# Optimization experiments

Measured on AMD Instinct MI355X. Metric: run time of the kernel, lower is better.

Reference implementation:

```python
import jax, jax.numpy as jnp
import numpy as np

B, S, C, H = 2, 2048, 2048, 16
Dh = C // H
ROPE_THETA = 10000.0


def _rope(t):
    # t: [B, S, H, Dh]; rotate-half RoPE over head_dim
    half = Dh // 2
    inv_freq = 1.0 / (ROPE_THETA ** (jnp.arange(0, half, dtype=jnp.float32) / half))
    ang = jnp.arange(S, dtype=jnp.float32)[:, None] * inv_freq[None, :]  # [S, half]
    cos = jnp.cos(ang)[None, :, None, :]  # [1,S,1,half]
    sin = jnp.sin(ang)[None, :, None, :]
    t1, t2 = t[..., :half], t[..., half:]
    return jnp.concatenate([t1 * cos - t2 * sin, t2 * cos + t1 * sin], axis=-1)


def setup_inputs() -> dict:
    key = jax.random.key(0)
    k1, k2, k3 = jax.random.split(key, 3)
    x = jax.random.normal(k1, (B, S, C), dtype=jnp.float32)
    Wqkv = jax.random.normal(k2, (C, 3 * C), dtype=jnp.float32) * (C ** -0.5)
    Wproj = jax.random.normal(k3, (C, C), dtype=jnp.float32) * (C ** -0.5)
    return {"x": x, "Wqkv": Wqkv, "Wproj": Wproj}


def reference(x, Wqkv, Wproj):
    batch, seq, hidden = x.shape
    qkv = x @ Wqkv  # [B,S,3C]
    # NOTE: torch code chunks as k, q, v (k first)
    k, q, v = jnp.split(qkv, 3, axis=-1)
    k = k.reshape(batch, seq, H, Dh)
    q = q.reshape(batch, seq, H, Dh)
    v = v.reshape(batch, seq, H, Dh)
    k = _rope(k)
    q = _rope(q)
    scale = Dh ** -0.5
    scores = jnp.einsum('bqhd,bkhd->bhqk', q, k) * scale  # [B,H,S,S]
    causal = jnp.tril(jnp.ones((seq, seq), dtype=bool))
    scores = jnp.where(causal[None, None], scores, jnp.finfo(scores.dtype).min)
    attn = jax.nn.softmax(scores, axis=-1)
    out = jnp.einsum('bhqk,bkhd->bqhd', attn, v).reshape(batch, seq, hidden)
    return out @ Wproj
```

## Files before the change

### kernel.cpp

```cpp
#include <hip/hip_runtime.h>
#include <hip/hip_bf16.h>

#define B_   2
#define S_   2048
#define C_   2048
#define H_   16
#define DH   128
#define C3   (3 * C_)

typedef __attribute__((ext_vector_type(8))) short short8;
typedef __attribute__((ext_vector_type(4))) float floatx4;

__device__ __forceinline__ void gload16(const void* g, void* l) {
  __builtin_amdgcn_global_load_lds(
      (const __attribute__((address_space(1))) unsigned int*)g,
      (__attribute__((address_space(3))) unsigned int*)l, 16, 0, 0);
}

__device__ __forceinline__ unsigned pk_bf16(float a, float b) {
  union { __hip_bfloat16 h; unsigned short u; } ua, ub;
  ua.h = __float2bfloat16(a); ub.h = __float2bfloat16(b);
  return (unsigned)ua.u | ((unsigned)ub.u << 16);
}

__global__ __launch_bounds__(256) void cast_bf16_kernel(
    const float* __restrict__ in, __hip_bfloat16* __restrict__ out, int n4) {
  int i = blockIdx.x * blockDim.x + threadIdx.x;
  if (i >= n4) return;
  float4 v = ((const float4*)in)[i];
  union { __hip_bfloat16 b[4]; uint2 u; } t;
  t.b[0] = __float2bfloat16(v.x);
  t.b[1] = __float2bfloat16(v.y);
  t.b[2] = __float2bfloat16(v.z);
  t.b[3] = __float2bfloat16(v.w);
  ((uint2*)out)[i] = t.u;
}

__global__ __launch_bounds__(256) void transpose_cast_kernel(
    const float* __restrict__ in, __hip_bfloat16* __restrict__ out, int R, int Cc) {
  __shared__ float tile[32][33];
  int c0 = blockIdx.x * 32, r0 = blockIdx.y * 32;
  int tx = threadIdx.x & 31, ty = threadIdx.x >> 5;
#pragma unroll
  for (int k = 0; k < 4; ++k)
    tile[ty + 8 * k][tx] = in[(size_t)(r0 + ty + 8 * k) * Cc + c0 + tx];
  __syncthreads();
#pragma unroll
  for (int k = 0; k < 4; ++k)
    out[(size_t)(c0 + ty + 8 * k) * R + r0 + tx] = __float2bfloat16(tile[tx][ty + 8 * k]);
}


#define S_VMCNT6 do { asm volatile("s_waitcnt vmcnt(6)" ::: "memory"); \
                      __builtin_amdgcn_sched_barrier(0); } while (0)
#define S_LGKM0  do { asm volatile("s_waitcnt lgkmcnt(0)" ::: "memory"); \
                      __builtin_amdgcn_sched_barrier(0); } while (0)
#define S_BAR    do { __builtin_amdgcn_s_barrier(); \
                      __builtin_amdgcn_sched_barrier(0); } while (0)

template <int NCOLS, bool OUT_F32>
__global__ __launch_bounds__(512, 2) void gemm_dp_kernel(
    const __hip_bfloat16* __restrict__ A, const __hip_bfloat16* __restrict__ Bt,
    void* __restrict__ Cp) {
  const int K = 2048, NT = 32;
  __shared__ __hip_bfloat16 lds[3 * 24576];
  const int tid = threadIdx.x;
  const int lane = tid & 63, wv = tid >> 6;
  const int wm = wv >> 1, wn = wv & 1;
  const int lr = lane & 15, lq = lane >> 4;
  const int m0 = blockIdx.y * 256, n0 = blockIdx.x * 128;
  const int sw0 = (lq ^ (lr & 7)) << 3;
  const int sw1 = sw0 ^ 32;

  auto stageA = [&](int bw, int p, int kk) {
    int idx = p * 512 + tid;
    int row = idx >> 3;
    int lc = (idx & 7) ^ (row & 7);
    gload16(A + (size_t)(m0 + row) * K + kk + lc * 8,
            (char*)lds + (size_t)bw * 49152 + (size_t)(p * 512 + wv * 64) * 16);
  };
  auto stageB = [&](int bw, int p, int kk) {
    int idx = p * 512 + tid;
    int row = idx >> 3;
    int lc = (idx & 7) ^ (row & 7);
    gload16(Bt + (size_t)(n0 + row) * K + kk + lc * 8,
            (char*)lds + (size_t)bw * 49152 + 32768 + (size_t)(p * 512 + wv * 64) * 16);
  };

#pragma unroll
  for (int p = 0; p < 4; ++p) stageA(0, p, 0);
#pragma unroll
  for (int p = 0; p < 2; ++p) stageB(0, p, 0);
#pragma unroll
  for (int p = 0; p < 4; ++p) stageA(1, p, 64);
#pragma unroll
  for (int p = 0; p < 2; ++p) stageB(1, p, 64);

  floatx4 acc[4][4] = {};
  int br = 0, bw = 2;

#pragma unroll 1
  for (int t = 0; t < NT; ++t) {
    const int kk2 = (t + 2 < NT) ? (t + 2) * 64 : 0;

    S_VMCNT6;
    S_BAR;

    const __hip_bfloat16* Ab = lds + br * 24576 + (wm * 64 + lr) * 64;
    const __hip_bfloat16* Bb = lds + br * 24576 + 16384 + (wn * 64 + lr) * 64;

    short8 af0[4], bf0[4];
#pragma unroll
    for (int i = 0; i < 4; ++i) af0[i] = *(const short8*)(Ab + i * 1024 + sw0);
#pragma unroll
    for (int j = 0; j < 4; ++j) bf0[j] = *(const short8*)(Bb + j * 1024 + sw0);
    stageA(bw, 0, kk2); stageA(bw, 1, kk2); stageB(bw, 0, kk2);
    S_LGKM0;
    __builtin_amdgcn_s_setprio(1);
#pragma unroll
    for (int i = 0; i < 4; ++i)
#pragma unroll
      for (int j = 0; j < 4; ++j)
        acc[i][j] = __builtin_amdgcn_mfma_f32_16x16x32_bf16(af0[i], bf0[j], acc[i][j], 0, 0, 0);
    __builtin_amdgcn_s_setprio(0);

    short8 af1[4], bf1[4];
#pragma unroll
    for (int i = 0; i < 4; ++i) af1[i] = *(const short8*)(Ab + i * 1024 + sw1);
#pragma unroll
    for (int j = 0; j < 4; ++j) bf1[j] = *(const short8*)(Bb + j * 1024 + sw1);
    stageA(bw, 2, kk2); stageA(bw, 3, kk2); stageB(bw, 1, kk2);
    S_LGKM0;
    __builtin_amdgcn_s_setprio(1);
#pragma unroll
    for (int i = 0; i < 4; ++i)
#pragma unroll
      for (int j = 0; j < 4; ++j)
        acc[i][j] = __builtin_amdgcn_mfma_f32_16x16x32_bf16(af1[i], bf1[j], acc[i][j], 0, 0, 0);
    __builtin_amdgcn_s_setprio(0);

    br = (br == 2) ? 0 : br + 1;
    bw = (bw == 2) ? 0 : bw + 1;
  }

  asm volatile("s_waitcnt vmcnt(0)" ::: "memory");
  __builtin_amdgcn_sched_barrier(0);

#pragma unroll
  for (int i = 0; i < 4; ++i)
#pragma unroll
    for (int j = 0; j < 4; ++j)
#pragma unroll
      for (int r = 0; r < 4; ++r) {
        int row = m0 + wm * 64 + i * 16 + lq * 4 + r;
        int col = n0 + wn * 64 + j * 16 + lr;
        if (OUT_F32)
          ((float*)Cp)[(size_t)row * NCOLS + col] = acc[i][j][r];
        else
          ((__hip_bfloat16*)Cp)[(size_t)row * NCOLS + col] = __float2bfloat16(acc[i][j][r]);
      }
}

__global__ __launch_bounds__(256) void rope_kernel(__hip_bfloat16* __restrict__ qkv) {
  int i = blockIdx.x * blockDim.x + threadIdx.x;
  int d = i & 63;
  int h = (i >> 6) & 15;
  int row = i >> 10;
  int s = row & (S_ - 1);
  float invf = exp2f((float)d * (-13.287712379549449f / 64.0f));
  float ang = (float)s * invf;
  float sn, c;
  __sincosf(ang, &sn, &c);
  size_t base = (size_t)row * C3 + h * DH + d;
  float k1 = __bfloat162float(qkv[base]);
  float k2 = __bfloat162float(qkv[base + 64]);
  qkv[base]      = __float2bfloat16(k1 * c - k2 * sn);
  qkv[base + 64] = __float2bfloat16(k2 * c + k1 * sn);
  const float scale = 0.08838834764831845f * 1.4426950408889634f;
  float q1 = __bfloat162float(qkv[base + C_]);
  float q2 = __bfloat162float(qkv[base + C_ + 64]);
  qkv[base + C_]      = __float2bfloat16((q1 * c - q2 * sn) * scale);
  qkv[base + C_ + 64] = __float2bfloat16((q2 * c + q1 * sn) * scale);
}

__global__ __launch_bounds__(256) void vtrans_kernel(
    const __hip_bfloat16* __restrict__ qkv, __hip_bfloat16* __restrict__ vt) {
  __shared__ short T[64 * 144];
  const int tid = threadIdx.x;
  const int t = blockIdx.x, bh = blockIdx.y;
  const int b = bh >> 4, h = bh & 15;
  const size_t brow = (size_t)b * S_;
#pragma unroll
  for (int p = 0; p < 4; ++p) {
    int idx = p * 256 + tid;
    int row = idx >> 4, c8 = idx & 15;
    *(short8*)(T + row * 144 + c8 * 8) =
        *(const short8*)(qkv + (brow + t * 64 + row) * C3 + 2 * C_ + h * DH + c8 * 8);
  }
  __syncthreads();
#pragma unroll
  for (int p = 0; p < 4; ++p) {
    int L = p * 256 + tid;
    int d = L & 127, cs = L >> 7;
    short8 v;
#pragma unroll
    for (int j = 0; j < 8; ++j) v[j] = T[(cs * 8 + j) * 144 + d];
    *(short8*)(vt + ((size_t)bh * 32 + t) * 8192 + (size_t)L * 8) = v;
  }
}

__global__ __launch_bounds__(256, 2) void attn_kernel(
    const __hip_bfloat16* __restrict__ qkv,
    const __hip_bfloat16* __restrict__ vt_tiles,
    __hip_bfloat16* __restrict__ outp) {
  __shared__ __hip_bfloat16 Ks[64 * 128];
  __shared__ __hip_bfloat16 Vt[64 * 128];
  __shared__ __hip_bfloat16 Ps[4 * 32 * 72];

  const int tid = threadIdx.x, lane = tid & 63, wv = tid >> 6;
  const int lr = lane & 15, lq = lane >> 4;
  const int qt = gridDim.x - 1 - blockIdx.x;
  const int bh = blockIdx.y;
  const int b = bh >> 4, h = bh & 15;
  const int q0 = qt * 128;
  const int q0w = q0 + wv * 32;
  const size_t brow = (size_t)b * S_;

  short8 qf[2][4];
#pragma unroll
  for (int rt = 0; rt < 2; ++rt)
#pragma unroll
    for (int ks = 0; ks < 4; ++ks)
      qf[rt][ks] = *(const short8*)(qkv + (brow + q0w + rt * 16 + lr) * C3 + C_ + h * DH + ks * 32 + lq * 8);

  floatx4 of[2][8] = {};
  float l_run[2] = {0.0f, 0.0f};

  const int wrow_last = q0w + 31;
  const int nkt = 2 * qt + 2;
  for (int kt = 0; kt < nkt; ++kt) {
    const int kb = kt * 64;
#pragma unroll
    for (int p = 0; p < 4; ++p) {
      int L = p * 256 + wv * 64 + lane;
      int srow = L >> 4;
      int ck = (L & 15) ^ (srow & 15);
      gload16(qkv + (brow + kb + srow) * C3 + h * DH + ck * 8,
              (char*)Ks + (size_t)(p * 256 + wv * 64) * 16);
      gload16(vt_tiles + ((size_t)bh * 32 + kt) * 8192 + (size_t)L * 8,
              (char*)Vt + (size_t)(p * 256 + wv * 64) * 16);
    }
    __syncthreads();

    if (kb <= wrow_last) {
      floatx4 st[2][4] = {};
#pragma unroll
      for (int ks = 0; ks < 4; ++ks) {
        short8 kfr[4];
#pragma unroll
        for (int t4 = 0; t4 < 4; ++t4)
          kfr[t4] = *(const short8*)(Ks + ((t4 * 16 + lr) * 16 + ((ks * 4 + lq) ^ lr)) * 8);
#pragma unroll
        for (int rt = 0; rt < 2; ++rt)
#pragma unroll
          for (int t4 = 0; t4 < 4; ++t4)
            st[rt][t4] = __builtin_amdgcn_mfma_f32_16x16x32_bf16(kfr[t4], qf[rt][ks], st[rt][t4], 0, 0, 0);
      }

      if (kb + 63 > q0w) {
#pragma unroll
        for (int rt = 0; rt < 2; ++rt)
#pragma unroll
          for (int t4 = 0; t4 < 4; ++t4)
#pragma unroll
            for (int r = 0; r < 4; ++r) {
              int s = kb + t4 * 16 + lq * 4 + r;
              if (s > q0w + rt * 16 + lr) st[rt][t4][r] = -1e30f;
            }
      }

#pragma unroll
      for (int rt = 0; rt < 2; ++rt) {
        float rs = 0.0f;
#pragma unroll
        for (int t4 = 0; t4 < 4; ++t4)
#pragma unroll
          for (int r = 0; r < 4; ++r) {
            float pv = exp2f(st[rt][t4][r]);
            st[rt][t4][r] = pv;
            rs += pv;
          }
        rs += __shfl_xor(rs, 16);
        rs += __shfl_xor(rs, 32);
        l_run[rt] += rs;
      }

#pragma unroll
      for (int rt = 0; rt < 2; ++rt)
#pragma unroll
        for (int t4 = 0; t4 < 4; ++t4) {
          unsigned* pdst = (unsigned*)(Ps + (wv * 32 + rt * 16 + lr) * 72 + t4 * 16 + lq * 4);
          pdst[0] = pk_bf16(st[rt][t4][0], st[rt][t4][1]);
          pdst[1] = pk_bf16(st[rt][t4][2], st[rt][t4][3]);
        }

#pragma unroll
      for (int ks = 0; ks < 2; ++ks) {
        short8 pa[2];
#pragma unroll
        for (int rt = 0; rt < 2; ++rt)
          pa[rt] = *(const short8*)(Ps + (wv * 32 + rt * 16 + lr) * 72 + ks * 32 + lq * 8);
#pragma unroll
        for (int dt = 0; dt < 8; ++dt) {
          short8 vb = *(const short8*)(Vt + ((ks * 4 + lq) * 128 + dt * 16 + lr) * 8);
#pragma unroll
          for (int rt = 0; rt < 2; ++rt)
            of[rt][dt] = __builtin_amdgcn_mfma_f32_16x16x32_bf16(pa[rt], vb, of[rt][dt], 0, 0, 0);
        }
      }
    }
    __syncthreads();
  }

#pragma unroll
  for (int rt = 0; rt < 2; ++rt) {
    float linv = 1.0f / l_run[rt];
    floatx4 lv;
#pragma unroll
    for (int r = 0; r < 4; ++r) lv[r] = __shfl(linv, lq * 4 + r);
#pragma unroll
    for (int dt = 0; dt < 8; ++dt)
#pragma unroll
      for (int r = 0; r < 4; ++r)
        outp[(brow + q0w + rt * 16 + lq * 4 + r) * C_ + h * DH + dt * 16 + lr] =
            __float2bfloat16(of[rt][dt][r] * lv[r]);
  }
}

extern "C" void kernel_launch(void* const* d_in, const int* in_sizes, int n_in,
                              void* d_out, int out_size, void* d_ws, size_t ws_size,
                              hipStream_t stream) {
  const float* x = (const float*)d_in[0];
  const float* Wqkv = (const float*)d_in[1];
  const float* Wproj = (const float*)d_in[2];

  __hip_bfloat16* xb = (__hip_bfloat16*)d_ws;
  __hip_bfloat16* WqkvT = xb + (size_t)4096 * 2048;
  __hip_bfloat16* qkvb = WqkvT + (size_t)6144 * 2048;
  __hip_bfloat16* WprojT = WqkvT;
  __hip_bfloat16* vt_tiles = WqkvT + (size_t)2048 * 2048;
  __hip_bfloat16* attnb = xb;

  cast_bf16_kernel<<<8192, 256, 0, stream>>>(x, xb, (4096 * 2048) / 4);
  transpose_cast_kernel<<<dim3(6144 / 32, 2048 / 32), 256, 0, stream>>>(Wqkv, WqkvT, 2048, 6144);

  gemm_dp_kernel<6144, false><<<dim3(6144 / 128, 4096 / 256), 512, 0, stream>>>(xb, WqkvT, qkvb);

  rope_kernel<<<(B_ * S_ * H_ * 64) / 256, 256, 0, stream>>>(qkvb);

  vtrans_kernel<<<dim3(32, 32), 256, 0, stream>>>(qkvb, vt_tiles);

  transpose_cast_kernel<<<dim3(2048 / 32, 2048 / 32), 256, 0, stream>>>(Wproj, WprojT, 2048, 2048);

  attn_kernel<<<dim3(16, 32), 256, 0, stream>>>(qkvb, vt_tiles, attnb);

  gemm_dp_kernel<2048, true><<<dim3(2048 / 128, 4096 / 256), 512, 0, stream>>>(
      attnb, WprojT, (float*)d_out);
}
```

Before: 378.8 us.

## Add dedicated QKV GEMM kernel with 256x192 tiles and interleaved double-buffered pipeline

Replaces the generic templated GEMM for the QKV projection with a specialized kernel using 256x192 block tiles, a 2x4 wave layout and 128x48 per-wave tiles. It double-buffers LDS and interleaves global-to-LDS loads with MFMA groups, using explicit waitcnt, barriers and setprio. The aim is more reuse per tile and a grid of 512 blocks that fills the CUs more evenly. The cost is larger register pressure from the 8x3 accumulators and more barriers per k-step, which could limit occupancy.

```diff
diff --git a/kernel.cpp b/kernel.cpp
--- a/kernel.cpp
+++ b/kernel.cpp
@@ -50,12 +50,157 @@
     out[(size_t)(c0 + ty + 8 * k) * R + r0 + tx] = __float2bfloat16(tile[tx][ty + 8 * k]);
 }
 
-
-#define S_VMCNT6 do { asm volatile("s_waitcnt vmcnt(6)" ::: "memory"); \
+#define S_VMCNT2 do { asm volatile("s_waitcnt vmcnt(2)" ::: "memory"); \
                       __builtin_amdgcn_sched_barrier(0); } while (0)
 #define S_LGKM0  do { asm volatile("s_waitcnt lgkmcnt(0)" ::: "memory"); \
                       __builtin_amdgcn_sched_barrier(0); } while (0)
 #define S_BAR    do { __builtin_amdgcn_s_barrier(); \
+                      __builtin_amdgcn_sched_barrier(0); } while (0)
+
+
+#define RD_A4(dst, buf, mh, sl)                                                          \
+  do {                                                                                   \
+    const __hip_bfloat16* base_ =                                                        \
+        lds + (buf) * 28672 + (wm * 128 + (mh) * 64 + lr) * 64 + ((sl) ? sw1 : sw0);     \
+    _Pragma("unroll") for (int i_ = 0; i_ < 4; ++i_)                                     \
+        dst[i_] = *(const short8*)(base_ + i_ * 1024);                                   \
+  } while (0)
+
+#define RD_B3(dst, buf, sl)                                                              \
+  do {                                                                                   \
+    const __hip_bfloat16* base_ =                                                        \
+        lds + (buf) * 28672 + 16384 + (wn * 48 + lr) * 64 + ((sl) ? sw1 : sw0);          \
+    _Pragma("unroll") for (int j_ = 0; j_ < 3; ++j_)                                     \
+        dst[j_] = *(const short8*)(base_ + j_ * 1024);                                   \
+  } while (0)
+
+#define MFG(afp, bfp, mh)                                                                \
+  do {                                                                                   \
+    __builtin_amdgcn_s_setprio(1);                                                       \
+    _Pragma("unroll") for (int i_ = 0; i_ < 4; ++i_)                                     \
+    _Pragma("unroll") for (int j_ = 0; j_ < 3; ++j_)                                     \
+        acc[(mh) * 4 + i_][j_] = __builtin_amdgcn_mfma_f32_16x16x32_bf16(                \
+            afp[i_], bfp[j_], acc[(mh) * 4 + i_][j_], 0, 0, 0);                          \
+    __builtin_amdgcn_s_setprio(0);                                                       \
+  } while (0)
+
+__global__ __launch_bounds__(512, 2) void gemm1_kernel(
+    const __hip_bfloat16* __restrict__ A, const __hip_bfloat16* __restrict__ Bt,
+    __hip_bfloat16* __restrict__ Cp) {
+  const int K = 2048;
+  __shared__ __hip_bfloat16 lds[2 * 28672];
+  const int tid = threadIdx.x;
+  const int lane = tid & 63, wv = tid >> 6;
+  const int wm = wv >> 2, wn = wv & 3;
+  const int lr = lane & 15, lq = lane >> 4;
+  const int m0 = blockIdx.y * 256, n0 = blockIdx.x * 192;
+  const int sw0 = (lq ^ (lr & 7)) << 3;
+  const int sw1 = sw0 ^ 32;
+
+  const __hip_bfloat16* Abase = A + (size_t)m0 * K;
+  const __hip_bfloat16* Bbase = Bt + (size_t)n0 * K;
+
+  auto stA = [&](int buf, int half, int kk) {
+#pragma unroll
+    for (int pp = 0; pp < 2; ++pp) {
+      int p = half * 2 + pp;
+      int idx = p * 512 + tid;
+      int row = idx >> 3;
+      int lc = (idx & 7) ^ (row & 7);
+      gload16(Abase + (size_t)row * K + kk + lc * 8,
+              (char*)lds + buf * 57344 + p * 8192 + wv * 1024);
+    }
+  };
+  auto stB2 = [&](int buf, int kk) {
+#pragma unroll
+    for (int p = 0; p < 2; ++p) {
+      int idx = p * 512 + tid;
+      int row = idx >> 3;
+      int lc = (idx & 7) ^ (row & 7);
+      gload16(Bbase + (size_t)row * K + kk + lc * 8,
+              (char*)lds + buf * 57344 + 32768 + p * 8192 + wv * 1024);
+    }
+  };
+  auto stB1 = [&](int buf, int kk) {
+    int idx = 2 * 512 + tid;
+    int row = idx >> 3;
+    int lc = (idx & 7) ^ (row & 7);
+    gload16(Bbase + (size_t)row * K + kk + lc * 8,
+            (char*)lds + buf * 57344 + 49152 + wv * 1024);
+  };
+
+  floatx4 acc[8][3] = {};
+  short8 afA[4], afB[4], afC[4], afD[4], bfA[3], bfB[3];
+
+  stA(0, 0, 0); stA(0, 1, 0); stB2(0, 0); stB1(0, 0);
+  stA(1, 0, 64);
+
+#pragma unroll 1
+  for (int it = 0; it < 16; ++it) {
+    const int t = 2 * it;
+    const int kk1 = (t + 1) * 64;
+    const int kk2 = (t + 2 < 32) ? (t + 2) * 64 : 0;
+    const int kk3 = (t + 3 < 32) ? (t + 3) * 64 : 0;
+
+    S_VMCNT2;
+    S_BAR;
+    RD_A4(afA, 0, 0, 0); RD_B3(bfA, 0, 0);
+    stA(1, 1, kk1);
+    S_LGKM0;
+    MFG(afA, bfA, 0);
+    S_BAR;
+    RD_A4(afB, 0, 1, 0); RD_A4(afC, 0, 0, 1);
+    stB2(1, kk1);
+    S_LGKM0;
+    MFG(afB, bfA, 1);
+    S_BAR;
+    RD_B3(bfB, 0, 1); RD_A4(afD, 0, 1, 1);
+    stB1(1, kk1);
+    S_LGKM0;
+    MFG(afC, bfB, 0);
+    S_BAR;
+    stA(0, 0, kk2);
+    MFG(afD, bfB, 1);
+    S_BAR;
+
+    S_VMCNT2;
+    S_BAR;
+    RD_A4(afA, 1, 0, 0); RD_B3(bfA, 1, 0);
+    stA(0, 1, kk2);
+    S_LGKM0;
+    MFG(afA, bfA, 0);
+    S_BAR;
+    RD_A4(afB, 1, 1, 0); RD_A4(afC, 1, 0, 1);
+    stB2(0, kk2);
+    S_LGKM0;
+    MFG(afB, bfA, 1);
+    S_BAR;
+    RD_B3(bfB, 1, 1); RD_A4(afD, 1, 1, 1);
+    stB1(0, kk2);
+    S_LGKM0;
+    MFG(afC, bfB, 0);
+    S_BAR;
+    stA(1, 0, kk3);
+    MFG(afD, bfB, 1);
+    S_BAR;
+  }
+
+  asm volatile("s_waitcnt vmcnt(0)" ::: "memory");
+  __builtin_amdgcn_sched_barrier(0);
+
+#pragma unroll
+  for (int i = 0; i < 8; ++i)
+#pragma unroll
+    for (int j = 0; j < 3; ++j)
+#pragma unroll
+      for (int r = 0; r < 4; ++r) {
+        int row = m0 + wm * 128 + i * 16 + lq * 4 + r;
+        int col = n0 + wn * 48 + j * 16 + lr;
+        Cp[(size_t)row * 6144 + col] = __float2bfloat16(acc[i][j][r]);
+      }
+}
+
+#define S_VMCNT6 do { asm volatile("s_waitcnt vmcnt(6)" ::: "memory"); \
                       __builtin_amdgcn_sched_barrier(0); } while (0)
 
 template <int NCOLS, bool OUT_F32>
@@ -354,7 +499,7 @@
   cast_bf16_kernel<<<8192, 256, 0, stream>>>(x, xb, (4096 * 2048) / 4);
   transpose_cast_kernel<<<dim3(6144 / 32, 2048 / 32), 256, 0, stream>>>(Wqkv, WqkvT, 2048, 6144);
 
-  gemm_dp_kernel<6144, false><<<dim3(6144 / 128, 4096 / 256), 512, 0, stream>>>(xb, WqkvT, qkvb);
+  gemm1_kernel<<<dim3(6144 / 192, 4096 / 256), 512, 0, stream>>>(xb, WqkvT, qkvb);
 
   rope_kernel<<<(B_ * S_ * H_ * 64) / 256, 256, 0, stream>>>(qkvb);
 
```

After: 373.6 us. About the same (-1.4%).
